# Optimization experiments

Measured on AMD Instinct MI355X. Metric: run time of the kernel, lower is better.

Reference implementation:

```python
import jax, jax.numpy as jnp
import numpy as np

IN_CH = 32
H = W = 512
NUM_CAMS = 4096
N_RAYS = 524288
HIDDEN = 128
ALPHA = 1e-4
# tensor_config = ['xy','xz','yz'] -> axis index pairs into t (x,y,z)
AXES = ((0, 1), (0, 2), (1, 2))


def grid_sample_border(plane, coords):
    """Bilinear grid_sample, padding_mode='border', align_corners=True.
    plane: (C,H,W); coords: (N,2) in [-1,1], coords[:,0]->W axis, coords[:,1]->H axis.
    Returns (N,C)."""
    C, Hh, Ww = plane.shape
    x = (coords[:, 0] + 1.0) * 0.5 * (Ww - 1)
    y = (coords[:, 1] + 1.0) * 0.5 * (Hh - 1)
    x0f = jnp.floor(x)
    y0f = jnp.floor(y)
    wx = (x - x0f)[None, :]
    wy = (y - y0f)[None, :]
    x0 = jnp.clip(x0f.astype(jnp.int32), 0, Ww - 1)
    x1 = jnp.clip(x0f.astype(jnp.int32) + 1, 0, Ww - 1)
    y0 = jnp.clip(y0f.astype(jnp.int32), 0, Hh - 1)
    y1 = jnp.clip(y0f.astype(jnp.int32) + 1, 0, Hh - 1)
    v00 = plane[:, y0, x0]  # (C,N)
    v01 = plane[:, y0, x1]
    v10 = plane[:, y1, x0]
    v11 = plane[:, y1, x1]
    out = (v00 * (1 - wx) * (1 - wy) + v01 * wx * (1 - wy)
           + v10 * (1 - wx) * wy + v11 * wx * wy)
    return out.T


def exp_so3(r):
    """Rodrigues: axis-angle (N,3) -> rotation matrices (N,3,3)."""
    theta = jnp.linalg.norm(r, axis=-1)[:, None, None]
    z = jnp.zeros_like(r[:, 0])
    K = jnp.stack([z, -r[:, 2], r[:, 1],
                   r[:, 2], z, -r[:, 0],
                   -r[:, 1], r[:, 0], z], axis=-1).reshape(-1, 3, 3)
    A = jnp.sin(theta) / (theta + 1e-10)
    B = (1.0 - jnp.cos(theta)) / (theta * theta + 1e-10)
    return jnp.eye(3, dtype=r.dtype) + A * K + B * (K @ K)


def setup_inputs() -> dict:
    key = jax.random.key(0)
    ks = jax.random.split(key, 12)
    cam_id = jax.random.randint(ks[0], (N_RAYS,), 0, NUM_CAMS, dtype=jnp.int32)
    t = jax.random.uniform(ks[1], (NUM_CAMS, 3), minval=-1.0, maxval=1.0, dtype=jnp.float32)
    plane_xy = jax.random.normal(ks[2], (IN_CH, H, W), dtype=jnp.float32)
    plane_xz = jax.random.normal(ks[3], (IN_CH, H, W), dtype=jnp.float32)
    plane_yz = jax.random.normal(ks[4], (IN_CH, H, W), dtype=jnp.float32)
    in_chs = IN_CH * 3
    # kaiming_normal_ init: std = sqrt(2/fan_in)
    w1 = jax.random.normal(ks[5], (in_chs, HIDDEN), dtype=jnp.float32) * np.sqrt(2.0 / in_chs)
    b1 = jax.random.normal(ks[6], (HIDDEN,), dtype=jnp.float32) * 0.01
    w2 = jax.random.normal(ks[7], (HIDDEN, HIDDEN), dtype=jnp.float32) * np.sqrt(2.0 / HIDDEN)
    b2 = jax.random.normal(ks[8], (HIDDEN,), dtype=jnp.float32) * 0.01
    w3 = jax.random.normal(ks[9], (HIDDEN, 3), dtype=jnp.float32) * np.sqrt(2.0 / HIDDEN)
    b3 = jax.random.normal(ks[10], (3,), dtype=jnp.float32) * 0.01
    top = jax.random.normal(ks[11], (NUM_CAMS, 3, 4), dtype=jnp.float32)
    bottom = jnp.tile(jnp.array([[[0.0, 0.0, 0.0, 1.0]]], dtype=jnp.float32), (NUM_CAMS, 1, 1))
    init_c2w = jnp.concatenate([top, bottom], axis=1)  # (NUM_CAMS,4,4)
    return {"cam_id": cam_id, "t": t, "plane_xy": plane_xy, "plane_xz": plane_xz,
            "plane_yz": plane_yz, "w1": w1, "b1": b1, "w2": w2, "b2": b2,
            "w3": w3, "b3": b3, "init_c2w": init_c2w}


def reference(cam_id, t, plane_xy, plane_xz, plane_yz, w1, b1, w2, b2, w3, b3, init_c2w):
    ts = t[cam_id]  # (N,3) per-ray translation
    coords_all = jax.lax.stop_gradient(ts)  # coords use t.data in the original
    codes = []
    for plane, (ax, ay) in zip((plane_xy, plane_xz, plane_yz), AXES):
        coords = jnp.stack([coords_all[:, ax], coords_all[:, ay]], axis=-1)
        codes.append(grid_sample_border(plane, coords))  # (N,IN_CH)
    codes = jnp.concatenate(codes, axis=-1)  # (N, 3*IN_CH)
    h = jax.nn.silu(codes @ w1 + b1)
    h = jax.nn.silu(h @ w2 + b2)
    rot = (h @ w3 + b3) * ALPHA  # (N,3) axis-angle
    R = exp_so3(rot)  # (N,3,3)
    c2w34 = jnp.concatenate([R, ts[:, :, None]], axis=-1)  # (N,3,4)
    bottom = jnp.broadcast_to(jnp.array([0.0, 0.0, 0.0, 1.0], dtype=c2w34.dtype),
                              (c2w34.shape[0], 1, 4))
    c2ws = jnp.concatenate([c2w34, bottom], axis=1)  # (N,4,4)
    return c2ws @ init_c2w[cam_id]
```

## Files before the change

kernel.cpp:

```cpp
#include <hip/hip_runtime.h>
#include <hip/hip_bf16.h>
#include <math.h>

#define HWDIM 512
#define HIDDEN 128
#define N_RAYS 524288
#define NUM_CAMS 4096
#define ALPHA 1e-4f

typedef __attribute__((ext_vector_type(4))) float f32x4;
typedef __attribute__((ext_vector_type(8))) short bf16x8;

__device__ __forceinline__ unsigned short f2bf(float f) {
    union { float f; unsigned u; } v; v.f = f;
    unsigned r = v.u + 0x7FFFu + ((v.u >> 16) & 1u);
    return (unsigned short)(r >> 16);
}
__device__ __forceinline__ float bf2f(unsigned short s) {
    union { unsigned u; float f; } v; v.u = ((unsigned)s) << 16;
    return v.f;
}

__global__ __launch_bounds__(256) void sample_kernel(
    const float* __restrict__ t,
    const float* __restrict__ pxy,
    const float* __restrict__ pxz,
    const float* __restrict__ pyz,
    unsigned short* __restrict__ codes)
{
    const int n = blockIdx.x * 256 + threadIdx.x;
    const int cam = n / 96;
    const int f = n - cam * 96;
    const int p = f >> 5;
    const int c = f & 31;

    const float ts0 = t[cam * 3 + 0];
    const float ts1 = t[cam * 3 + 1];
    const float ts2 = t[cam * 3 + 2];

    const float* plane;
    float cx, cy;
    if (p == 0)      { plane = pxy; cx = ts0; cy = ts1; }
    else if (p == 1) { plane = pxz; cx = ts0; cy = ts2; }
    else             { plane = pyz; cx = ts1; cy = ts2; }

    const float x = (cx + 1.0f) * 0.5f * (float)(HWDIM - 1);
    const float y = (cy + 1.0f) * 0.5f * (float)(HWDIM - 1);
    const float x0f = floorf(x);
    const float y0f = floorf(y);
    const float wx = x - x0f;
    const float wy = y - y0f;
    const int x0 = min(max((int)x0f, 0), HWDIM - 1);
    const int x1 = min(max((int)x0f + 1, 0), HWDIM - 1);
    const int y0 = min(max((int)y0f, 0), HWDIM - 1);
    const int y1 = min(max((int)y0f + 1, 0), HWDIM - 1);

    const float* pc = plane + (size_t)c * (HWDIM * HWDIM);
    const float v00 = pc[y0 * HWDIM + x0];
    const float v01 = pc[y0 * HWDIM + x1];
    const float v10 = pc[y1 * HWDIM + x0];
    const float v11 = pc[y1 * HWDIM + x1];

    const float val = v00 * (1.0f - wx) * (1.0f - wy)
                    + v01 * wx          * (1.0f - wy)
                    + v10 * (1.0f - wx) * wy
                    + v11 * wx          * wy;
    codes[n] = f2bf(val);
}

#define W1S 104
#define W2S 136
#define HS  136

__global__ __launch_bounds__(256) void mlp_kernel(
    const unsigned short* __restrict__ codes,
    const float* __restrict__ t,
    const float* __restrict__ w1, const float* __restrict__ b1,
    const float* __restrict__ w2, const float* __restrict__ b2,
    const float* __restrict__ w3, const float* __restrict__ b3,
    const float* __restrict__ init_c2w,
    float* __restrict__ table)
{
    const int tid  = threadIdx.x;
    const int lane = tid & 63;
    const int wave = tid >> 6;
    const int cam0 = blockIdx.x * 16;
    const int ncol = lane & 15;
    const int kgrp = lane >> 4;

    __shared__ unsigned short w1t[128][W1S];
    __shared__ unsigned short w2t[128][W2S];
    __shared__ unsigned short h1t[16][HS];
    __shared__ unsigned short h2t[16][HS];
    __shared__ float b1s[128], b2s[128], w3s[384];
    __shared__ float rotc[16][3];
    __shared__ float c2ws[16][12];

    for (int i = tid; i < 96 * 128; i += 256) {
        const int k = i >> 7, n = i & 127;
        w1t[n][k] = f2bf(w1[i]);
    }
    for (int i = tid; i < 128 * 128; i += 256) {
        const int k = i >> 7, n = i & 127;
        w2t[n][k] = f2bf(w2[i]);
    }
    if (tid < 128) { b1s[tid] = b1[tid]; b2s[tid] = b2[tid]; }
    for (int i = tid; i < 384; i += 256) w3s[i] = w3[i];
    __syncthreads();

    const int nb0 = wave * 32 + ncol;
    const int nb1 = nb0 + 16;

    f32x4 acc0, acc1;
    {
        const float bv0 = b1s[nb0], bv1 = b1s[nb1];
        acc0 = (f32x4){bv0, bv0, bv0, bv0};
        acc1 = (f32x4){bv1, bv1, bv1, bv1};
    }
    const unsigned short* arow = codes + (size_t)(cam0 + ncol) * 96;
    #pragma unroll
    for (int k0 = 0; k0 < 96; k0 += 32) {
        const bf16x8 a   = *reinterpret_cast<const bf16x8*>(arow + k0 + kgrp * 8);
        const bf16x8 bb0 = *reinterpret_cast<const bf16x8*>(&w1t[nb0][k0 + kgrp * 8]);
        const bf16x8 bb1 = *reinterpret_cast<const bf16x8*>(&w1t[nb1][k0 + kgrp * 8]);
        acc0 = __builtin_amdgcn_mfma_f32_16x16x32_bf16(a, bb0, acc0, 0, 0, 0);
        acc1 = __builtin_amdgcn_mfma_f32_16x16x32_bf16(a, bb1, acc1, 0, 0, 0);
    }
    #pragma unroll
    for (int r = 0; r < 4; ++r) {
        const int camr = kgrp * 4 + r;
        const float v0 = acc0[r];
        const float v1 = acc1[r];
        h1t[camr][nb0] = f2bf(v0 / (1.0f + __expf(-v0)));
        h1t[camr][nb1] = f2bf(v1 / (1.0f + __expf(-v1)));
    }
    __syncthreads();

    {
        const float bv0 = b2s[nb0], bv1 = b2s[nb1];
        acc0 = (f32x4){bv0, bv0, bv0, bv0};
        acc1 = (f32x4){bv1, bv1, bv1, bv1};
    }
    #pragma unroll
    for (int k0 = 0; k0 < 128; k0 += 32) {
        const bf16x8 a   = *reinterpret_cast<const bf16x8*>(&h1t[ncol][k0 + kgrp * 8]);
        const bf16x8 bb0 = *reinterpret_cast<const bf16x8*>(&w2t[nb0][k0 + kgrp * 8]);
        const bf16x8 bb1 = *reinterpret_cast<const bf16x8*>(&w2t[nb1][k0 + kgrp * 8]);
        acc0 = __builtin_amdgcn_mfma_f32_16x16x32_bf16(a, bb0, acc0, 0, 0, 0);
        acc1 = __builtin_amdgcn_mfma_f32_16x16x32_bf16(a, bb1, acc1, 0, 0, 0);
    }
    #pragma unroll
    for (int r = 0; r < 4; ++r) {
        const int camr = kgrp * 4 + r;
        const float v0 = acc0[r];
        const float v1 = acc1[r];
        h2t[camr][nb0] = f2bf(v0 / (1.0f + __expf(-v0)));
        h2t[camr][nb1] = f2bf(v1 / (1.0f + __expf(-v1)));
    }
    __syncthreads();

    if (tid < 64) {
        const int cam = tid >> 2, c = tid & 3;
        if (c < 3) {
            float acc = b3[c];
            for (int k = 0; k < 128; ++k)
                acc += bf2f(h2t[cam][k]) * w3s[k * 3 + c];
            rotc[cam][c] = acc * ALPHA;
        }
    }
    __syncthreads();

    if (tid < 16) {
        const int cam = tid;
        const float a = rotc[cam][0], b = rotc[cam][1], c = rotc[cam][2];
        const float th2 = a * a + b * b + c * c;
        const float th = sqrtf(th2);
        const float A = sinf(th) / (th + 1e-10f);
        const float B = (1.0f - cosf(th)) / (th2 + 1e-10f);
        const float ts0 = t[(cam0 + cam) * 3 + 0];
        const float ts1 = t[(cam0 + cam) * 3 + 1];
        const float ts2 = t[(cam0 + cam) * 3 + 2];
        c2ws[cam][0]  = 1.0f + B * (-(c * c + b * b));
        c2ws[cam][1]  = A * (-c) + B * (a * b);
        c2ws[cam][2]  = A * b + B * (a * c);
        c2ws[cam][3]  = ts0;
        c2ws[cam][4]  = A * c + B * (a * b);
        c2ws[cam][5]  = 1.0f + B * (-(c * c + a * a));
        c2ws[cam][6]  = A * (-a) + B * (b * c);
        c2ws[cam][7]  = ts1;
        c2ws[cam][8]  = A * (-b) + B * (a * c);
        c2ws[cam][9]  = A * a + B * (b * c);
        c2ws[cam][10] = 1.0f + B * (-(a * a + b * b));
        c2ws[cam][11] = ts2;
    }
    __syncthreads();

    {
        const int cam = tid >> 4, e = tid & 15, i = e >> 2, j = e & 3;
        const float* ic = init_c2w + (size_t)(cam0 + cam) * 16;
        float v;
        if (i < 3) {
            const float* cw = c2ws[cam];
            v = cw[i * 4 + 0] * ic[0 + j]
              + cw[i * 4 + 1] * ic[4 + j]
              + cw[i * 4 + 2] * ic[8 + j]
              + cw[i * 4 + 3] * ic[12 + j];
        } else {
            v = ic[12 + j];
        }
        table[(size_t)cam0 * 16 + tid] = v;
    }
}

__global__ __launch_bounds__(256) void gather_kernel(
    const int* __restrict__ cam_id,
    const float4* __restrict__ table,
    float4* __restrict__ out)
{
    const int idx = blockIdx.x * blockDim.x + threadIdx.x;
    if (idx >= N_RAYS * 4) return;
    const int ray = idx >> 2;
    const int q = idx & 3;
    const int cid = cam_id[ray];
    out[idx] = table[cid * 4 + q];
}

extern "C" void kernel_launch(void* const* d_in, const int* in_sizes, int n_in,
                              void* d_out, int out_size, void* d_ws, size_t ws_size,
                              hipStream_t stream) {
    const int*   cam_id   = (const int*)  d_in[0];
    const float* t        = (const float*)d_in[1];
    const float* pxy      = (const float*)d_in[2];
    const float* pxz      = (const float*)d_in[3];
    const float* pyz      = (const float*)d_in[4];
    const float* w1       = (const float*)d_in[5];
    const float* b1       = (const float*)d_in[6];
    const float* w2       = (const float*)d_in[7];
    const float* b2       = (const float*)d_in[8];
    const float* w3       = (const float*)d_in[9];
    const float* b3       = (const float*)d_in[10];
    const float* init_c2w = (const float*)d_in[11];

    float* table = (float*)d_ws;
    unsigned short* codes = (unsigned short*)((char*)d_ws + NUM_CAMS * 16 * 4);

    sample_kernel<<<(NUM_CAMS * 96) / 256, 256, 0, stream>>>(t, pxy, pxz, pyz, codes);

    mlp_kernel<<<NUM_CAMS / 16, 256, 0, stream>>>(
        codes, t, w1, b1, w2, b2, w3, b3, init_c2w, table);

    const int total = N_RAYS * 4;
    gather_kernel<<<(total + 255) / 256, 256, 0, stream>>>(
        cam_id, (const float4*)table, (float4*)d_out);
}
```

Before: 42.46 us.

## Fuse plane sampling into MLP kernel and pre-convert weights once

The bilinear plane sampling now runs inside the per-camera MLP kernel and writes codes straight to shared memory, so the global codes buffer and one kernel launch are gone. A small prep kernel converts and transposes w1/w2 to bf16 once in global memory. Each MLP block no longer rebuilds the full transposed weights in LDS and instead reads B fragments from global or L2. Blocks grow to 512 threads with one 16-column tile per wave, which trades LDS traffic and per-block setup for uncached global weight reads.

Measured after the change: 38.90 us. 1.09x faster.

```diff
diff --git a/kernel.cpp b/kernel.cpp
--- a/kernel.cpp
+++ b/kernel.cpp
@@ -21,62 +21,28 @@
     return v.f;
 }
 
-__global__ __launch_bounds__(256) void sample_kernel(
+__global__ __launch_bounds__(256) void prep_kernel(
+    const float* __restrict__ w1, const float* __restrict__ w2,
+    unsigned short* __restrict__ w1T, unsigned short* __restrict__ w2T)
+{
+    const int idx = blockIdx.x * 256 + threadIdx.x;
+    if (idx < 96 * 128) {
+        const int k = idx >> 7, n = idx & 127;
+        w1T[n * 96 + k] = f2bf(w1[idx]);
+    } else {
+        const int j = idx - 96 * 128;
+        const int k = j >> 7, n = j & 127;
+        w2T[n * 128 + k] = f2bf(w2[j]);
+    }
+}
+
+__global__ __launch_bounds__(512) void fused_kernel(
     const float* __restrict__ t,
     const float* __restrict__ pxy,
     const float* __restrict__ pxz,
     const float* __restrict__ pyz,
-    unsigned short* __restrict__ codes)
-{
-    const int n = blockIdx.x * 256 + threadIdx.x;
-    const int cam = n / 96;
-    const int f = n - cam * 96;
-    const int p = f >> 5;
-    const int c = f & 31;
-
-    const float ts0 = t[cam * 3 + 0];
-    const float ts1 = t[cam * 3 + 1];
-    const float ts2 = t[cam * 3 + 2];
-
-    const float* plane;
-    float cx, cy;
-    if (p == 0)      { plane = pxy; cx = ts0; cy = ts1; }
-    else if (p == 1) { plane = pxz; cx = ts0; cy = ts2; }
-    else             { plane = pyz; cx = ts1; cy = ts2; }
-
-    const float x = (cx + 1.0f) * 0.5f * (float)(HWDIM - 1);
-    const float y = (cy + 1.0f) * 0.5f * (float)(HWDIM - 1);
-    const float x0f = floorf(x);
-    const float y0f = floorf(y);
-    const float wx = x - x0f;
-    const float wy = y - y0f;
-    const int x0 = min(max((int)x0f, 0), HWDIM - 1);
-    const int x1 = min(max((int)x0f + 1, 0), HWDIM - 1);
-    const int y0 = min(max((int)y0f, 0), HWDIM - 1);
-    const int y1 = min(max((int)y0f + 1, 0), HWDIM - 1);
-
-    const float* pc = plane + (size_t)c * (HWDIM * HWDIM);
-    const float v00 = pc[y0 * HWDIM + x0];
-    const float v01 = pc[y0 * HWDIM + x1];
-    const float v10 = pc[y1 * HWDIM + x0];
-    const float v11 = pc[y1 * HWDIM + x1];
-
-    const float val = v00 * (1.0f - wx) * (1.0f - wy)
-                    + v01 * wx          * (1.0f - wy)
-                    + v10 * (1.0f - wx) * wy
-                    + v11 * wx          * wy;
-    codes[n] = f2bf(val);
-}
-
-#define W1S 104
-#define W2S 136
-#define HS  136
-
-__global__ __launch_bounds__(256) void mlp_kernel(
-    const unsigned short* __restrict__ codes,
-    const float* __restrict__ t,
-    const float* __restrict__ w1, const float* __restrict__ b1,
-    const float* __restrict__ w2, const float* __restrict__ b2,
+    const unsigned short* __restrict__ w1T, const float* __restrict__ b1,
+    const unsigned short* __restrict__ w2T, const float* __restrict__ b2,
     const float* __restrict__ w3, const float* __restrict__ b3,
     const float* __restrict__ init_c2w,
     float* __restrict__ table)
@@ -88,84 +54,94 @@
     const int ncol = lane & 15;
     const int kgrp = lane >> 4;
 
-    __shared__ unsigned short w1t[128][W1S];
-    __shared__ unsigned short w2t[128][W2S];
-    __shared__ unsigned short h1t[16][HS];
-    __shared__ unsigned short h2t[16][HS];
-    __shared__ float b1s[128], b2s[128], w3s[384];
+    __shared__ unsigned short h0t[16][104];
+    __shared__ unsigned short h1t[16][136];
+    __shared__ unsigned short h2t[16][136];
+    __shared__ float w3s[384];
     __shared__ float rotc[16][3];
     __shared__ float c2ws[16][12];
 
-    for (int i = tid; i < 96 * 128; i += 256) {
-        const int k = i >> 7, n = i & 127;
-        w1t[n][k] = f2bf(w1[i]);
-    }
-    for (int i = tid; i < 128 * 128; i += 256) {
-        const int k = i >> 7, n = i & 127;
-        w2t[n][k] = f2bf(w2[i]);
-    }
-    if (tid < 128) { b1s[tid] = b1[tid]; b2s[tid] = b2[tid]; }
-    for (int i = tid; i < 384; i += 256) w3s[i] = w3[i];
-    __syncthreads();
-
-    const int nb0 = wave * 32 + ncol;
-    const int nb1 = nb0 + 16;
-
-    f32x4 acc0, acc1;
-    {
-        const float bv0 = b1s[nb0], bv1 = b1s[nb1];
-        acc0 = (f32x4){bv0, bv0, bv0, bv0};
-        acc1 = (f32x4){bv1, bv1, bv1, bv1};
-    }
-    const unsigned short* arow = codes + (size_t)(cam0 + ncol) * 96;
+    #pragma unroll
+    for (int j = 0; j < 3; ++j) {
+        const int task = tid + 512 * j;
+        const int cl = task / 96;
+        const int f = task - cl * 96;
+        const int p = f >> 5;
+        const int c = f & 31;
+        const int cam = cam0 + cl;
+
+        const float ts0 = t[cam * 3 + 0];
+        const float ts1 = t[cam * 3 + 1];
+        const float ts2 = t[cam * 3 + 2];
+        const float cx = (p == 2) ? ts1 : ts0;
+        const float cy = (p == 0) ? ts1 : ts2;
+        const float* plane = (p == 0) ? pxy : ((p == 1) ? pxz : pyz);
+
+        const float x = (cx + 1.0f) * 0.5f * (float)(HWDIM - 1);
+        const float y = (cy + 1.0f) * 0.5f * (float)(HWDIM - 1);
+        const float x0f = floorf(x);
+        const float y0f = floorf(y);
+        const float wx = x - x0f;
+        const float wy = y - y0f;
+        const int x0 = min(max((int)x0f, 0), HWDIM - 1);
+        const int x1 = min(max((int)x0f + 1, 0), HWDIM - 1);
+        const int y0 = min(max((int)y0f, 0), HWDIM - 1);
+        const int y1 = min(max((int)y0f + 1, 0), HWDIM - 1);
+
+        const float* pc = plane + (size_t)c * (HWDIM * HWDIM);
+        const float v00 = pc[y0 * HWDIM + x0];
+        const float v01 = pc[y0 * HWDIM + x1];
+        const float v10 = pc[y1 * HWDIM + x0];
+        const float v11 = pc[y1 * HWDIM + x1];
+
+        const float val = v00 * (1.0f - wx) * (1.0f - wy)
+                        + v01 * wx          * (1.0f - wy)
+                        + v10 * (1.0f - wx) * wy
+                        + v11 * wx          * wy;
+        h0t[cl][f] = f2bf(val);
+    }
+    if (tid < 384) w3s[tid] = w3[tid];
+    __syncthreads();
+
+    const int nb = wave * 16 + ncol;
+    f32x4 acc;
+    { const float bv = b1[nb]; acc = (f32x4){bv, bv, bv, bv}; }
     #pragma unroll
     for (int k0 = 0; k0 < 96; k0 += 32) {
-        const bf16x8 a   = *reinterpret_cast<const bf16x8*>(arow + k0 + kgrp * 8);
-        const bf16x8 bb0 = *reinterpret_cast<const bf16x8*>(&w1t[nb0][k0 + kgrp * 8]);
-        const bf16x8 bb1 = *reinterpret_cast<const bf16x8*>(&w1t[nb1][k0 + kgrp * 8]);
-        acc0 = __builtin_amdgcn_mfma_f32_16x16x32_bf16(a, bb0, acc0, 0, 0, 0);
-        acc1 = __builtin_amdgcn_mfma_f32_16x16x32_bf16(a, bb1, acc1, 0, 0, 0);
+        const bf16x8 a  = *reinterpret_cast<const bf16x8*>(&h0t[ncol][k0 + kgrp * 8]);
+        const bf16x8 bb = *reinterpret_cast<const bf16x8*>(w1T + nb * 96 + k0 + kgrp * 8);
+        acc = __builtin_amdgcn_mfma_f32_16x16x32_bf16(a, bb, acc, 0, 0, 0);
     }
     #pragma unroll
     for (int r = 0; r < 4; ++r) {
         const int camr = kgrp * 4 + r;
-        const float v0 = acc0[r];
-        const float v1 = acc1[r];
-        h1t[camr][nb0] = f2bf(v0 / (1.0f + __expf(-v0)));
-        h1t[camr][nb1] = f2bf(v1 / (1.0f + __expf(-v1)));
-    }
-    __syncthreads();
-
-    {
-        const float bv0 = b2s[nb0], bv1 = b2s[nb1];
-        acc0 = (f32x4){bv0, bv0, bv0, bv0};
-        acc1 = (f32x4){bv1, bv1, bv1, bv1};
-    }
+        const float v = acc[r];
+        h1t[camr][nb] = f2bf(v / (1.0f + __expf(-v)));
+    }
+    __syncthreads();
+
+    { const float bv = b2[nb]; acc = (f32x4){bv, bv, bv, bv}; }
     #pragma unroll
     for (int k0 = 0; k0 < 128; k0 += 32) {
-        const bf16x8 a   = *reinterpret_cast<const bf16x8*>(&h1t[ncol][k0 + kgrp * 8]);
-        const bf16x8 bb0 = *reinterpret_cast<const bf16x8*>(&w2t[nb0][k0 + kgrp * 8]);
-        const bf16x8 bb1 = *reinterpret_cast<const bf16x8*>(&w2t[nb1][k0 + kgrp * 8]);
-        acc0 = __builtin_amdgcn_mfma_f32_16x16x32_bf16(a, bb0, acc0, 0, 0, 0);
-        acc1 = __builtin_amdgcn_mfma_f32_16x16x32_bf16(a, bb1, acc1, 0, 0, 0);
+        const bf16x8 a  = *reinterpret_cast<const bf16x8*>(&h1t[ncol][k0 + kgrp * 8]);
+        const bf16x8 bb = *reinterpret_cast<const bf16x8*>(w2T + nb * 128 + k0 + kgrp * 8);
+        acc = __builtin_amdgcn_mfma_f32_16x16x32_bf16(a, bb, acc, 0, 0, 0);
     }
     #pragma unroll
     for (int r = 0; r < 4; ++r) {
         const int camr = kgrp * 4 + r;
-        const float v0 = acc0[r];
-        const float v1 = acc1[r];
-        h2t[camr][nb0] = f2bf(v0 / (1.0f + __expf(-v0)));
-        h2t[camr][nb1] = f2bf(v1 / (1.0f + __expf(-v1)));
+        const float v = acc[r];
+        h2t[camr][nb] = f2bf(v / (1.0f + __expf(-v)));
     }
     __syncthreads();
 
     if (tid < 64) {
         const int cam = tid >> 2, c = tid & 3;
         if (c < 3) {
-            float acc = b3[c];
+            float a3 = b3[c];
             for (int k = 0; k < 128; ++k)
-                acc += bf2f(h2t[cam][k]) * w3s[k * 3 + c];
-            rotc[cam][c] = acc * ALPHA;
+                a3 += bf2f(h2t[cam][k]) * w3s[k * 3 + c];
+            rotc[cam][c] = a3 * ALPHA;
         }
     }
     __syncthreads();
@@ -195,7 +171,7 @@
     }
     __syncthreads();
 
-    {
+    if (tid < 256) {
         const int cam = tid >> 4, e = tid & 15, i = e >> 2, j = e & 3;
         const float* ic = init_c2w + (size_t)(cam0 + cam) * 16;
         float v;
@@ -241,14 +217,14 @@
     const float* b3       = (const float*)d_in[10];
     const float* init_c2w = (const float*)d_in[11];
 
-    float* table = (float*)d_ws;
-    unsigned short* codes = (unsigned short*)((char*)d_ws + NUM_CAMS * 16 * 4);
-
-    sample_kernel<<<(NUM_CAMS * 96) / 256, 256, 0, stream>>>(t, pxy, pxz, pyz, codes);
-
-    mlp_kernel<<<NUM_CAMS / 16, 256, 0, stream>>>(
-        codes, t, w1, b1, w2, b2, w3, b3, init_c2w, table);
-
+    char* ws = (char*)d_ws;
+    float* table = (float*)ws;
+    unsigned short* w1T = (unsigned short*)(ws + 262144);
+    unsigned short* w2T = (unsigned short*)(ws + 262144 + 24576);
+
+    prep_kernel<<<112, 256, 0, stream>>>(w1, w2, w1T, w2T);
+    fused_kernel<<<NUM_CAMS / 16, 512, 0, stream>>>(
+        t, pxy, pxz, pyz, w1T, b1, w2T, b2, w3, b3, init_c2w, table);
     const int total = N_RAYS * 4;
     gather_kernel<<<(total + 255) / 256, 256, 0, stream>>>(
         cam_id, (const float4*)table, (float4*)d_out);
```
